# Kernel optimization log

Hardware: AMD Instinct MI355X
Metric: run time of the kernel (lower is better)

## Reference

```python
import jax, jax.numpy as jnp
import numpy as np

B, T, S = 32, 32, 400
H, E = 512, 300
V, MAX_OOV = 45000, 50
EXT_V = V + MAX_OOV
NEG = 1.0e12  # INF constant from the torch module


def setup_inputs() -> dict:
    key = jax.random.key(0)
    ks = jax.random.split(key, 16)
    p = lambda k, shape: jax.random.normal(k, shape, jnp.float32) * 0.02
    ext = jax.random.randint(ks[0], (B, S), 0, EXT_V, dtype=jnp.int64 if jax.config.jax_enable_x64 else jnp.int32)
    ext = ext.at[0, 0].set(EXT_V - 1)  # pin max OOV id so num_oov == MAX_OOV (matches torch data-dependent size)
    return {
        "trg_seq_embedded": jax.random.normal(ks[1], (B, T, E), jnp.float32),
        "ext_src_seq": ext,
        "init_states": jax.random.normal(ks[2], (1, B, H), jnp.float32),
        "encoder_outputs": jax.random.normal(ks[3], (B, S, H), jnp.float32),
        "encoder_mask": jnp.ones((B, S), jnp.int32),
        "W_enc": p(ks[4], (H, H)), "b_enc": jnp.zeros((H,), jnp.float32),
        "W_red": p(ks[5], (E, E + H)), "b_red": jnp.zeros((E,), jnp.float32),
        "W_ih": p(ks[6], (4 * H, E)), "W_hh": p(ks[7], (4 * H, H)),
        "b_ih": jnp.zeros((4 * H,), jnp.float32), "b_hh": jnp.zeros((4 * H,), jnp.float32),
        "W_cat": p(ks[8], (H, 2 * H)), "b_cat": jnp.zeros((H,), jnp.float32),
        "W_log": p(ks[9], (V, H)), "b_log": jnp.zeros((V,), jnp.float32),
    }


def reference(trg_seq_embedded, ext_src_seq, init_states, encoder_outputs, encoder_mask,
              W_enc, b_enc, W_red, b_red, W_ih, W_hh, b_ih, b_hh, W_cat, b_cat, W_log, b_log):
    batch = trg_seq_embedded.shape[0]
    # encoder features (memories): [B, S, H]
    memories = jnp.einsum('bsh,gh->bsg', encoder_outputs, W_enc) + b_enc
    batch_idx = jnp.arange(batch)[:, None]
    bias = b_ih + b_hh

    def step(carry, emb):
        h, c, ctx, cov = carry
        # reduce_layer on [embedded ; prev_context] -> [B, E]
        x = jnp.concatenate([emb, ctx], axis=-1) @ W_red.T + b_red
        # single-layer LSTM cell, torch gate order i,f,g,o
        gates = x @ W_ih.T + h @ W_hh.T + bias
        i_g, f_g, g_g, o_g = jnp.split(gates, 4, axis=-1)
        c_new = jax.nn.sigmoid(f_g) * c + jax.nn.sigmoid(i_g) * jnp.tanh(g_g)
        h_new = jax.nn.sigmoid(o_g) * jnp.tanh(c_new)
        # Bahdanau-style dot attention
        energy = jnp.einsum('bh,bsh->bs', h_new, memories)
        energy = jnp.where(encoder_mask == 0, -NEG, energy)
        attn = jax.nn.softmax(energy, axis=1)
        context = jnp.einsum('bs,bsh->bh', attn, memories)
        # output projection
        logit_in = jnp.tanh(jnp.concatenate([h_new, context], axis=-1) @ W_cat.T + b_cat)
        logit = logit_in @ W_log.T + b_log  # [B, V]
        # pointer: scatter_max of energies into extended vocabulary
        ext_logit = jnp.concatenate([logit, jnp.zeros((batch, EXT_V - V), logit.dtype)], axis=1)
        out = jnp.full((batch, EXT_V), -NEG, logit.dtype).at[batch_idx, ext_src_seq].max(energy)
        out = jnp.where(out == -NEG, 0.0, out)
        logit2 = ext_logit + out
        logit2 = jnp.where(logit2 == 0.0, -NEG, logit2)
        return (h_new, c_new, context, cov + attn), (logit2, attn, cov, energy)

    h0 = init_states[0]
    carry0 = (h0, h0, jnp.zeros((batch, memories.shape[-1]), trg_seq_embedded.dtype),
              jnp.zeros((batch, memories.shape[1]), trg_seq_embedded.dtype))
    _, (logits, attn_out, cov_out, energies) = jax.lax.scan(
        step, carry0, jnp.swapaxes(trg_seq_embedded, 0, 1))
    # each stacked over time: logits [T,B,EXT_V], attn/coverage/energies [T,B,S]
    return logits, attn_out, cov_out, energies
```

## Files before the change

kernel.cpp:

```cpp
#include <hip/hip_runtime.h>
#include <hip/hip_bf16.h>

typedef _Float16 h2 __attribute__((ext_vector_type(2)));
typedef _Float16 h8 __attribute__((ext_vector_type(8)));
typedef __attribute__((ext_vector_type(4))) float floatx4;

#define NEGF 1.0e12f

#if __has_builtin(__builtin_amdgcn_fdot2)
#define DOT2(a,b,c) __builtin_amdgcn_fdot2((a),(b),(c),false)
#else
static __device__ __forceinline__ float DOT2(h2 a, h2 b, float c){
  return c + (float)a[0]*(float)b[0] + (float)a[1]*(float)b[1];
}
#endif

__device__ __forceinline__ float dot8(h8 a, h8 b, float c){
  h2 a0 = {a[0],a[1]}, a1 = {a[2],a[3]}, a2 = {a[4],a[5]}, a3 = {a[6],a[7]};
  h2 b0 = {b[0],b[1]}, b1 = {b[2],b[3]}, b2 = {b[4],b[5]}, b3 = {b[6],b[7]};
  c = DOT2(a0,b0,c); c = DOT2(a1,b1,c); c = DOT2(a2,b2,c); c = DOT2(a3,b3,c);
  return c;
}

__device__ __forceinline__ unsigned f16bits(float x){
  union { _Float16 h; unsigned short u; } cv; cv.h = (_Float16)x; return (unsigned)cv.u;
}

#define GLD_LDS16(g, l) __builtin_amdgcn_global_load_lds( \
    (const __attribute__((address_space(1))) void*)(g),   \
    (__attribute__((address_space(3))) void*)(l), 16, 0, 0)

#define ALOAD64(p)    __hip_atomic_load((p), __ATOMIC_RELAXED, __HIP_MEMORY_SCOPE_AGENT)
#define ASTORE32(p,v) __hip_atomic_store((p), (v), __ATOMIC_RELAXED, __HIP_MEMORY_SCOPE_AGENT)

template<int EPI>
__global__ __launch_bounds__(256) void gemm_f16(
    const _Float16* __restrict__ A, const _Float16* __restrict__ B,
    float* __restrict__ Cf, _Float16* __restrict__ Ch,
    const float* __restrict__ bias, int N, int K, int ldc, int ntn)
{
  __shared__ char smem[32768];
  _Float16* Al = (_Float16*)smem;
  _Float16* Bl = (_Float16*)(smem + 16384);
  int bid = blockIdx.x;
  int bn = bid % ntn, bm = bid / ntn;
  int t = threadIdx.x;
  int w = t >> 6, l = t & 63;

  floatx4 acc[4][4];
#pragma unroll
  for (int i = 0; i < 4; ++i)
#pragma unroll
    for (int j = 0; j < 4; ++j) acc[i][j] = (floatx4){0.f, 0.f, 0.f, 0.f};

  const char* Ab = (const char*)A + (size_t)bm * 128 * K * 2;
  const char* Bb = (const char*)B + (size_t)bn * 128 * K * 2;
  const int rowb = K * 2;
  const int r0 = t >> 3;
  const int cbyte = ((t & 7) * 16) ^ (((t >> 3) & 7) << 4);
  char* AlB = (char*)Al;
  char* BlB = (char*)Bl;
  const int wm = (w >> 1) * 64, wn = (w & 1) * 64;

  for (int kt = 0; kt < K; kt += 64) {
    __syncthreads();
#pragma unroll
    for (int c = 0; c < 4; ++c) {
      int row = c * 32 + r0;
      GLD_LDS16(Ab + (size_t)row * rowb + kt * 2 + cbyte, AlB + c * 4096 + t * 16);
      GLD_LDS16(Bb + (size_t)row * rowb + kt * 2 + cbyte, BlB + c * 4096 + t * 16);
    }
    __syncthreads();
#pragma unroll
    for (int kk = 0; kk < 64; kk += 32) {
      h8 af[4], bfv[4];
#pragma unroll
      for (int i = 0; i < 4; ++i) {
        int ra = wm + i * 16 + (l & 15);
        int cb = ((kk << 1) + ((l >> 4) << 4)) ^ ((ra & 7) << 4);
        af[i] = *(const h8*)(AlB + ra * 128 + cb);
      }
#pragma unroll
      for (int j = 0; j < 4; ++j) {
        int ra = wn + j * 16 + (l & 15);
        int cb = ((kk << 1) + ((l >> 4) << 4)) ^ ((ra & 7) << 4);
        bfv[j] = *(const h8*)(BlB + ra * 128 + cb);
      }
#pragma unroll
      for (int i = 0; i < 4; ++i)
#pragma unroll
        for (int j = 0; j < 4; ++j)
          acc[i][j] = __builtin_amdgcn_mfma_f32_16x16x32_f16(af[i], bfv[j], acc[i][j], 0, 0, 0);
    }
  }

  if (EPI == 3) {
    float* Cs = (float*)smem;
#pragma unroll
    for (int half = 0; half < 2; ++half) {
      __syncthreads();
      if ((w >> 1) == half) {
        int rbase = ((l >> 4) << 2);
#pragma unroll
        for (int i = 0; i < 4; ++i)
#pragma unroll
          for (int j = 0; j < 4; ++j)
#pragma unroll
            for (int r = 0; r < 4; ++r)
              Cs[(i * 16 + rbase + r) * 128 + wn + j * 16 + (l & 15)] = acc[i][j][r];
      }
      __syncthreads();
#pragma unroll
      for (int rr = 0; rr < 16; ++rr) {
        int row = rr * 4 + w;
        int grow = bm * 128 + half * 64 + row;
        int cc = bn * 128 + 2 * l;
        float2 v = *(float2*)&Cs[row * 128 + 2 * l];
        float vv0, vv1;
        if (cc < N)     { float x0 = v.x + bias[cc];     vv0 = (x0 == 0.f) ? -NEGF : x0; } else vv0 = -NEGF;
        if (cc + 1 < N) { float x1 = v.y + bias[cc + 1]; vv1 = (x1 == 0.f) ? -NEGF : x1; } else vv1 = -NEGF;
        float* orow = Cf + (size_t)grow * ldc;
        if (cc + 1 < ldc) { float2 o; o.x = vv0; o.y = vv1; *(float2*)(orow + cc) = o; }
        else if (cc < ldc) orow[cc] = vv0;
      }
    }
  } else {
    int mbase = bm * 128 + wm + ((l >> 4) << 2);
    int nbase = bn * 128 + wn + (l & 15);
#pragma unroll
    for (int j = 0; j < 4; ++j) {
      int col = nbase + j * 16;
#pragma unroll
      for (int i = 0; i < 4; ++i) {
#pragma unroll
        for (int r = 0; r < 4; ++r) {
          int row = mbase + i * 16 + r;
          float v = acc[i][j][r];
          if (col < N) {
            float bv = bias ? bias[col] : 0.f;
            if (EPI == 0)      Cf[(size_t)row * ldc + col] = v + bv;
            else if (EPI == 1) Ch[(size_t)row * ldc + col] = (_Float16)(v + bv);
            else               Ch[(size_t)row * ldc + col] = (_Float16)tanhf(v + bv);
          }
        }
      }
    }
  }
}

__global__ void cast_pad_kernel(const float* __restrict__ src, _Float16* __restrict__ dst,
                                int R, int C, int ld_src, int Cpad, int ld_dst, long total){
  long i = (long)blockIdx.x * 256 + threadIdx.x;
  if (i >= total) return;
  int r = (int)(i / Cpad), c = (int)(i % Cpad);
  float v = (r < R && c < C) ? src[(size_t)r * ld_src + c] : 0.f;
  dst[(size_t)r * ld_dst + c] = (_Float16)v;
}

__global__ void cast_emb_kernel(const float* __restrict__ trg, _Float16* __restrict__ dst){
  int i = blockIdx.x * 256 + threadIdx.x;
  if (i >= 1024 * 320) return;
  int m = i / 320, e = i % 320;
  int tt = m >> 5, b = m & 31;
  float v = (e < 300) ? trg[((size_t)b * 32 + tt) * 300 + e] : 0.f;
  dst[i] = (_Float16)v;
}

__global__ void cast_wr2t_kernel(const float* __restrict__ wred, _Float16* __restrict__ dst){
  int i = blockIdx.x * 256 + threadIdx.x;
  if (i >= 512 * 320) return;
  int h = i / 320, e = i % 320;
  float v = (e < 300) ? wred[(size_t)e * 812 + 300 + h] : 0.f;
  dst[i] = (_Float16)v;
}

__global__ void init_kernel(const float* __restrict__ h0, const float* __restrict__ b_ih,
                            const float* __restrict__ b_hh,
                            _Float16* __restrict__ HCzT, float* __restrict__ bias_sum,
                            _Float16* __restrict__ X1h, unsigned* __restrict__ bar){
  int i = blockIdx.x * 256 + threadIdx.x;
  if (i < 32768) {
    int unit = i >> 3, pos = i & 7;
    int kc = unit >> 5, b = unit & 31;
    int k = kc * 8 + pos;
    HCzT[i] = (k < 512) ? (_Float16)h0[b * 512 + k] : (_Float16)0.f;
  }
  if (i < 2048)  bias_sum[i] = b_ih[i] + b_hh[i];
  if (i < 327680) X1h[i] = (_Float16)0.f;
  if (i < 1024) bar[i] = 0u;
}

__device__ __forceinline__ void gbar(unsigned* cnt){
  asm volatile("s_waitcnt vmcnt(0)" ::: "memory");
  __syncthreads();
  if (threadIdx.x == 0) {
    __hip_atomic_fetch_add(cnt, 1u, __ATOMIC_RELAXED, __HIP_MEMORY_SCOPE_AGENT);
    while (__hip_atomic_load(cnt, __ATOMIC_RELAXED, __HIP_MEMORY_SCOPE_AGENT) < 32u)
      __builtin_amdgcn_s_sleep(1);
  }
  __syncthreads();
  asm volatile("" ::: "memory");
}

__global__ __launch_bounds__(512, 1) void fused_loop(
    const _Float16* __restrict__ memh, _Float16* __restrict__ HCzT,
    _Float16* __restrict__ HC_A, const _Float16* __restrict__ Wz,
    const float* __restrict__ P, const float* __restrict__ inits,
    const int* __restrict__ mask, float* __restrict__ e_out,
    float* __restrict__ a_out, float* __restrict__ c_out, unsigned* __restrict__ bar)
{
  __shared__ char smem[32768];
  __shared__ float es[400];
  __shared__ float red[16];
  __shared__ float cum[400];
  __shared__ _Float16 hh[512];

  float* gl = (float*)smem;
  const int q = blockIdx.x, t = threadIdx.x;
  const int w = t >> 6, l = t & 63;
  const int mw = w >> 2, nw = w & 3;

  if (t < 400) cum[t] = 0.f;

  float creg = inits[(t >> 4) * 512 + q * 16 + (t & 15)];
  const _Float16* mb = memh + (size_t)q * 400 * 512;

  const _Float16* wbase[4];
#pragma unroll
  for (int s = 0; s < 4; ++s)
    wbase[s] = Wz + (size_t)(s * 512 + q * 16 + (l & 15)) * 1024 + nw * 256 + ((l >> 4) << 3);

  __syncthreads();

  for (int ts = 0; ts < 32; ++ts) {
    {
      unsigned long long* zsrc = (unsigned long long*)(HCzT + (size_t)ts * 32768);
      floatx4 acc[4];
#pragma unroll
      for (int s = 0; s < 4; ++s) acc[s] = (floatx4){0.f, 0.f, 0.f, 0.f};
#pragma unroll
      for (int kk8 = 0; kk8 < 8; ++kk8) {
        int unit = ((nw * 8 + kk8) * 4 + (l >> 4)) * 32 + mw * 16 + (l & 15);
        union { unsigned long long u[2]; h8 v; } za;
        za.u[0] = ALOAD64(zsrc + (size_t)unit * 2);
        za.u[1] = ALOAD64(zsrc + (size_t)unit * 2 + 1);
#pragma unroll
        for (int s = 0; s < 4; ++s) {
          h8 wv = *(const h8*)(wbase[s] + kk8 * 32);
          acc[s] = __builtin_amdgcn_mfma_f32_16x16x32_f16(za.v, wv, acc[s], 0, 0, 0);
        }
      }
#pragma unroll
      for (int s = 0; s < 4; ++s)
#pragma unroll
        for (int r = 0; r < 4; ++r) {
          int b = mw * 16 + ((l >> 4) << 2) + r;
          gl[(s * 4 + nw) * 512 + b * 16 + (l & 15)] = acc[s][r];
        }
    }
    __syncthreads();
    {
      int b = t >> 4, j16 = t & 15;
      const float* Pr = P + ((size_t)ts * 32 + b) * 2048 + q * 16 + j16;
      float g4[4];
#pragma unroll
      for (int s = 0; s < 4; ++s)
        g4[s] = gl[(s * 4 + 0) * 512 + t] + gl[(s * 4 + 1) * 512 + t]
              + gl[(s * 4 + 2) * 512 + t] + gl[(s * 4 + 3) * 512 + t] + Pr[s * 512];
      float ig = 1.f / (1.f + expf(-g4[0]));
      float fg = 1.f / (1.f + expf(-g4[1]));
      float og = 1.f / (1.f + expf(-g4[3]));
      float cn = fg * creg + ig * tanhf(g4[2]);
      float hn = og * tanhf(cn);
      creg = cn;
      unsigned hu = f16bits(hn);
      unsigned other = __shfl_xor(hu, 1);
      if (!(t & 1)) {
        unsigned pack = hu | (other << 16);
        int j = q * 16 + j16;
        unsigned* dst = (unsigned*)((char*)(HCzT + (size_t)(ts + 1) * 32768)
                                    + (((j >> 3) * 32 + b) << 4) + ((j & 7) << 1));
        ASTORE32(dst, pack);
        *(unsigned*)(HC_A + ((size_t)ts * 32 + b) * 1024 + j) = pack;
      }
    }
    gbar(bar + ts * 32);

    size_t obase = (size_t)ts * 12800 + q * 400;
    {
      if (t < 64) {
        unsigned long long* hsrc = (unsigned long long*)(HCzT + (size_t)(ts + 1) * 32768);
        union { unsigned long long u[2]; h8 v; } ha;
        ha.u[0] = ALOAD64(hsrc + ((size_t)t * 32 + q) * 2);
        ha.u[1] = ALOAD64(hsrc + ((size_t)t * 32 + q) * 2 + 1);
        *(h8*)&hh[t * 8] = ha.v;
      }
      __syncthreads();

      {
        int g = l >> 2, c = l & 3;
#pragma unroll
        for (int r = 0; r < 4; ++r) {
          int sr = r * 16 + g;
          if (sr < 50) {
            int s = w * 50 + sr;
            const _Float16* row = mb + (size_t)s * 512 + c * 128;
            float e = 0.f;
#pragma unroll
            for (int k = 0; k < 16; ++k)
              e = dot8(*(const h8*)(row + k * 8), *(const h8*)&hh[c * 128 + k * 8], e);
            e += __shfl_xor(e, 1);
            e += __shfl_xor(e, 2);
            if (c == 0) {
              if (mask[q * 400 + s] == 0) e = -NEGF;
              es[s] = e;
            }
          }
        }
      }
      __syncthreads();
      if (t < 400) e_out[obase + t] = es[t];

      float v = (t < 400) ? es[t] : -3.4e38f;
      float m = v;
#pragma unroll
      for (int o = 32; o; o >>= 1) m = fmaxf(m, __shfl_xor(m, o));
      if (l == 0) red[w] = m;
      __syncthreads();
      m = red[0];
#pragma unroll
      for (int qq = 1; qq < 8; ++qq) m = fmaxf(m, red[qq]);
      float p = (t < 400) ? expf(v - m) : 0.f;
      float sum = p;
#pragma unroll
      for (int o = 32; o; o >>= 1) sum += __shfl_xor(sum, o);
      if (l == 0) red[8 + w] = sum;
      __syncthreads();
      float tot = red[8];
#pragma unroll
      for (int qq = 9; qq < 16; ++qq) tot += red[qq];
      float inv = 1.f / tot;
      float aval = p * inv;
      if (t < 400) {
        es[t] = aval;
        a_out[obase + t] = aval;
        c_out[obase + t] = cum[t];
        cum[t] += aval;
      }
      __syncthreads();

      float acc2 = 0.f;
#pragma unroll 4
      for (int s = 0; s < 400; ++s)
        acc2 += es[s] * (float)mb[(size_t)s * 512 + t];
      unsigned cu = f16bits(acc2);
      unsigned other = __shfl_xor(cu, 1);
      if (!(t & 1)) {
        unsigned pack = cu | (other << 16);
        int kg = 512 + t;
        unsigned* dst = (unsigned*)((char*)(HCzT + (size_t)(ts + 1) * 32768)
                                    + (((kg >> 3) * 32 + q) << 4) + ((kg & 7) << 1));
        ASTORE32(dst, pack);
        *(unsigned*)(HC_A + ((size_t)ts * 32 + q) * 1024 + kg) = pack;
      }
    }
    gbar(bar + ts * 32 + 16);
  }
}

__global__ __launch_bounds__(512) void pointer_kernel(
    const int* __restrict__ ext, const float* __restrict__ energ, float* __restrict__ logits)
{
  __shared__ int ids[400];
  __shared__ float es[400];
  int tb = blockIdx.x;
  int b = tb & 31;
  int tt = tb >> 5;
  int t = threadIdx.x;
  if (t < 400) {
    ids[t] = ext[b * 400 + t];
    es[t] = energ[(size_t)tt * 12800 + b * 400 + t];
  }
  __syncthreads();
  if (t < 400) {
    int id = ids[t];
    bool first = true;
    for (int s = 0; s < t; ++s) if (ids[s] == id) { first = false; break; }
    if (first) {
      float mx = es[t];
      for (int s = t + 1; s < 400; ++s) if (ids[s] == id) mx = fmaxf(mx, es[s]);
      if (mx != -NEGF) {
        float* p = &logits[(size_t)tb * 45050 + id];
        float base = 0.f;
        if (id < 45000) { float cur = *p; base = (cur == -NEGF) ? 0.f : cur; }
        float nv = base + mx;
        *p = (nv == 0.f) ? -NEGF : nv;
      }
    }
  }
}

extern "C" void kernel_launch(void* const* d_in, const int* in_sizes, int n_in,
                              void* d_out, int out_size, void* d_ws, size_t ws_size,
                              hipStream_t stream) {
  const float* trg   = (const float*)d_in[0];
  const int*   ext   = (const int*)d_in[1];
  const float* inits = (const float*)d_in[2];
  const float* enc   = (const float*)d_in[3];
  const int*   mask  = (const int*)d_in[4];
  const float* W_enc = (const float*)d_in[5];
  const float* b_enc = (const float*)d_in[6];
  const float* W_red = (const float*)d_in[7];
  const float* b_red = (const float*)d_in[8];
  const float* W_ih  = (const float*)d_in[9];
  const float* W_hh  = (const float*)d_in[10];
  const float* b_ih  = (const float*)d_in[11];
  const float* b_hh  = (const float*)d_in[12];
  const float* W_cat = (const float*)d_in[13];
  const float* b_cat = (const float*)d_in[14];
  const float* W_log = (const float*)d_in[15];
  const float* b_log = (const float*)d_in[16];

  float* out = (float*)d_out;
  float* out_logits = out;
  float* out_attn   = out + 46131200;
  float* out_cov    = out_attn + 409600;
  float* out_energy = out_cov + 409600;

  char* ws = (char*)d_ws;
  size_t o = 0;
  auto alloc = [&](size_t bytes) { void* p = ws + o; o += (bytes + 255) & ~(size_t)255; return p; };
  _Float16* mem_h   = (_Float16*)alloc(12800ULL * 512 * 2);
  _Float16* enc_h   = (_Float16*)alloc(12800ULL * 512 * 2);
  _Float16* W_enc_h = (_Float16*)alloc(512ULL * 512 * 2);
  _Float16* emb_h   = (_Float16*)alloc(1024ULL * 320 * 2);
  _Float16* Wr1_h   = (_Float16*)alloc(384ULL * 320 * 2);
  _Float16* X1_h    = (_Float16*)alloc(1024ULL * 320 * 2);
  _Float16* W_ih_h  = (_Float16*)alloc(2048ULL * 320 * 2);
  _Float16* Wr2T_h  = (_Float16*)alloc(512ULL * 320 * 2);
  _Float16* W_cat_h = (_Float16*)alloc(512ULL * 1024 * 2);
  _Float16* W_log_h = (_Float16*)alloc(45056ULL * 512 * 2);
  _Float16* A_log_h = (_Float16*)alloc(1024ULL * 512 * 2);
  _Float16* HCzT    = (_Float16*)alloc(33ULL * 32768 * 2);
  _Float16* HC_A    = (_Float16*)alloc(1024ULL * 1024 * 2);
  _Float16* Wz      = (_Float16*)alloc(2048ULL * 1024 * 2);
  float* P        = (float*)alloc(1024ULL * 2048 * 4);
  float* bias_sum = (float*)alloc(2048ULL * 4);
  unsigned* bar   = (unsigned*)alloc(4096);

  auto blocks = [](long total) { return (int)((total + 255) / 256); };

  init_kernel<<<blocks(327680), 256, 0, stream>>>(inits, b_ih, b_hh, HCzT, bias_sum, X1_h, bar);
  cast_pad_kernel<<<blocks(12800L*512), 256, 0, stream>>>(enc,   enc_h,   12800, 512, 512, 512, 512, 12800L*512);
  cast_pad_kernel<<<blocks(512L*512),   256, 0, stream>>>(W_enc, W_enc_h, 512,   512, 512, 512, 512, 512L*512);
  cast_pad_kernel<<<blocks(384L*320),   256, 0, stream>>>(W_red, Wr1_h,   300,   300, 812, 320, 320, 384L*320);
  cast_pad_kernel<<<blocks(2048L*320),  256, 0, stream>>>(W_ih,  W_ih_h,  2048,  300, 300, 320, 320, 2048L*320);
  cast_pad_kernel<<<blocks(512L*1024),  256, 0, stream>>>(W_cat, W_cat_h, 512,  1024, 1024, 1024, 1024, 512L*1024);
  cast_pad_kernel<<<blocks(45056L*512), 256, 0, stream>>>(W_log, W_log_h, 45000, 512, 512, 512, 512, 45056L*512);
  cast_pad_kernel<<<blocks(2048L*512),  256, 0, stream>>>(W_hh,  Wz,      2048,  512, 512, 512, 1024, 2048L*512);
  cast_emb_kernel<<<blocks(1024L*320), 256, 0, stream>>>(trg, emb_h);
  cast_wr2t_kernel<<<blocks(512L*320), 256, 0, stream>>>(W_red, Wr2T_h);

  gemm_f16<1><<<400, 256, 0, stream>>>(enc_h, W_enc_h, nullptr, mem_h, b_enc, 512, 512, 512, 4);
  gemm_f16<1><<<24,  256, 0, stream>>>(emb_h, Wr1_h, nullptr, X1_h, b_red, 300, 320, 320, 3);
  gemm_f16<0><<<128, 256, 0, stream>>>(X1_h, W_ih_h, P, nullptr, bias_sum, 2048, 320, 2048, 16);
  gemm_f16<1><<<64,  256, 0, stream>>>(W_ih_h, Wr2T_h, nullptr, Wz + 512, nullptr, 512, 320, 1024, 4);

  fused_loop<<<32, 512, 0, stream>>>(mem_h, HCzT, HC_A, Wz, P, inits, mask,
                                     out_energy, out_attn, out_cov, bar);

  gemm_f16<2><<<32, 256, 0, stream>>>(HC_A, W_cat_h, nullptr, A_log_h, b_cat, 512, 1024, 512, 4);
  gemm_f16<3><<<2816, 256, 0, stream>>>(A_log_h, W_log_h, out_logits, nullptr, b_log, 45000, 512, 45050, 352);
  pointer_kernel<<<1024, 512, 0, stream>>>(ext, out_energy, out_logits);
}
```

Before: 1.393 ms.

## Transpose encoder memories for vectorized context reduction and use flag-based grid barrier

Adds a transpose kernel that writes the encoder memories in [b][h][s] layout, reusing the enc_h buffer. Each thread in the recurrent loop can then compute the attention context with contiguous 16-byte loads and vectorized shared-memory reads, instead of strided scalar loads. The grid barrier moves from a single atomic counter to per-block generation flags, polled in parallel by one wavefront with a ballot, to shorten barrier latency. The cost is one extra transpose launch and more global reads per barrier poll.

```diff
diff --git a/kernel.cpp b/kernel.cpp
--- a/kernel.cpp
+++ b/kernel.cpp
@@ -174,6 +174,34 @@
   dst[i] = (_Float16)v;
 }
 
+__global__ __launch_bounds__(256) void transpose_mem(
+    const _Float16* __restrict__ src, _Float16* __restrict__ dst)
+{
+  __shared__ _Float16 tile[64][66];
+  int bid = blockIdx.x;
+  int b = bid / 56, rem = bid % 56;
+  int st = rem / 8, dt = rem % 8;
+  int t = threadIdx.x;
+  int lane = t & 63, grp = t >> 6;
+  const _Float16* s0 = src + (size_t)b * 400 * 512;
+#pragma unroll
+  for (int j = 0; j < 16; ++j) {
+    int sl = grp * 16 + j;
+    int s = st * 64 + sl;
+    if (s < 400) tile[sl][lane] = s0[(size_t)s * 512 + dt * 64 + lane];
+  }
+  __syncthreads();
+  _Float16* d0 = dst + (size_t)b * 512 * 400;
+  int s = st * 64 + lane;
+  if (s < 400) {
+#pragma unroll
+    for (int j = 0; j < 16; ++j) {
+      int dl = grp * 16 + j;
+      d0[(size_t)(dt * 64 + dl) * 400 + s] = tile[lane][dl];
+    }
+  }
+}
+
 __global__ void init_kernel(const float* __restrict__ h0, const float* __restrict__ b_ih,
                             const float* __restrict__ b_hh,
                             _Float16* __restrict__ HCzT, float* __restrict__ bias_sum,
@@ -190,27 +218,33 @@
   if (i < 1024) bar[i] = 0u;
 }
 
-__device__ __forceinline__ void gbar(unsigned* cnt){
+__device__ __forceinline__ void gbar2(unsigned* flags, unsigned gen){
   asm volatile("s_waitcnt vmcnt(0)" ::: "memory");
   __syncthreads();
-  if (threadIdx.x == 0) {
-    __hip_atomic_fetch_add(cnt, 1u, __ATOMIC_RELAXED, __HIP_MEMORY_SCOPE_AGENT);
-    while (__hip_atomic_load(cnt, __ATOMIC_RELAXED, __HIP_MEMORY_SCOPE_AGENT) < 32u)
-      __builtin_amdgcn_s_sleep(1);
+  if (threadIdx.x < 64) {
+    if (threadIdx.x == 0)
+      __hip_atomic_store(flags + blockIdx.x, gen, __ATOMIC_RELAXED, __HIP_MEMORY_SCOPE_AGENT);
+    for (;;) {
+      unsigned v = (threadIdx.x < 32)
+        ? __hip_atomic_load(flags + threadIdx.x, __ATOMIC_RELAXED, __HIP_MEMORY_SCOPE_AGENT)
+        : gen;
+      if (__ballot(v >= gen) == ~0ULL) break;
+    }
   }
   __syncthreads();
   asm volatile("" ::: "memory");
 }
 
 __global__ __launch_bounds__(512, 1) void fused_loop(
-    const _Float16* __restrict__ memh, _Float16* __restrict__ HCzT,
-    _Float16* __restrict__ HC_A, const _Float16* __restrict__ Wz,
-    const float* __restrict__ P, const float* __restrict__ inits,
-    const int* __restrict__ mask, float* __restrict__ e_out,
-    float* __restrict__ a_out, float* __restrict__ c_out, unsigned* __restrict__ bar)
+    const _Float16* __restrict__ memh, const _Float16* __restrict__ memT,
+    _Float16* __restrict__ HCzT, _Float16* __restrict__ HC_A,
+    const _Float16* __restrict__ Wz, const float* __restrict__ P,
+    const float* __restrict__ inits, const int* __restrict__ mask,
+    float* __restrict__ e_out, float* __restrict__ a_out,
+    float* __restrict__ c_out, unsigned* __restrict__ bar)
 {
   __shared__ char smem[32768];
-  __shared__ float es[400];
+  __shared__ __align__(16) float es[400];
   __shared__ float red[16];
   __shared__ float cum[400];
   __shared__ _Float16 hh[512];
@@ -224,6 +258,7 @@
 
   float creg = inits[(t >> 4) * 512 + q * 16 + (t & 15)];
   const _Float16* mb = memh + (size_t)q * 400 * 512;
+  const _Float16* rowT = memT + (size_t)q * 204800 + (size_t)t * 400;
 
   const _Float16* wbase[4];
 #pragma unroll
@@ -284,7 +319,7 @@
         *(unsigned*)(HC_A + ((size_t)ts * 32 + b) * 1024 + j) = pack;
       }
     }
-    gbar(bar + ts * 32);
+    gbar2(bar, ts + 1);
 
     size_t obase = (size_t)ts * 12800 + q * 400;
     {
@@ -350,9 +385,16 @@
       __syncthreads();
 
       float acc2 = 0.f;
-#pragma unroll 4
-      for (int s = 0; s < 400; ++s)
-        acc2 += es[s] * (float)mb[(size_t)s * 512 + t];
+#pragma unroll
+      for (int si = 0; si < 50; ++si) {
+        h8 mv = *(const h8*)(rowT + si * 8);
+        float4 ea = *(const float4*)&es[si * 8];
+        float4 eb = *(const float4*)&es[si * 8 + 4];
+        acc2 += ea.x * (float)mv[0] + ea.y * (float)mv[1]
+              + ea.z * (float)mv[2] + ea.w * (float)mv[3]
+              + eb.x * (float)mv[4] + eb.y * (float)mv[5]
+              + eb.z * (float)mv[6] + eb.w * (float)mv[7];
+      }
       unsigned cu = f16bits(acc2);
       unsigned other = __shfl_xor(cu, 1);
       if (!(t & 1)) {
@@ -364,7 +406,7 @@
         *(unsigned*)(HC_A + ((size_t)ts * 32 + q) * 1024 + kg) = pack;
       }
     }
-    gbar(bar + ts * 32 + 16);
+    gbar2(bar + 32, ts + 1);
   }
 }
 
@@ -447,6 +489,7 @@
   float* P        = (float*)alloc(1024ULL * 2048 * 4);
   float* bias_sum = (float*)alloc(2048ULL * 4);
   unsigned* bar   = (unsigned*)alloc(4096);
+  _Float16* memT  = enc_h;
 
   auto blocks = [](long total) { return (int)((total + 255) / 256); };
 
@@ -466,7 +509,9 @@
   gemm_f16<0><<<128, 256, 0, stream>>>(X1_h, W_ih_h, P, nullptr, bias_sum, 2048, 320, 2048, 16);
   gemm_f16<1><<<64,  256, 0, stream>>>(W_ih_h, Wr2T_h, nullptr, Wz + 512, nullptr, 512, 320, 1024, 4);
 
-  fused_loop<<<32, 512, 0, stream>>>(mem_h, HCzT, HC_A, Wz, P, inits, mask,
+  transpose_mem<<<32 * 56, 256, 0, stream>>>(mem_h, memT);
+
+  fused_loop<<<32, 512, 0, stream>>>(mem_h, memT, HCzT, HC_A, Wz, P, inits, mask,
                                      out_energy, out_attn, out_cov, bar);
 
   gemm_f16<2><<<32, 256, 0, stream>>>(HC_A, W_cat_h, nullptr, A_log_h, b_cat, 512, 1024, 512, 4);
```

New measurement: 1.647 ms. 18.3% more time.

## Replace grid-barrier LSTM split with per-batch blocks computing full gates

Applied to the files above, without the earlier changes.

Restructures the recurrent loop so each block handles one batch element and computes all LSTM gates locally with fp16 dot products over a repacked weight layout. This removes the two grid-wide atomic barriers per timestep and the global h/context exchange buffer. In exchange, every block streams the full recurrent weight matrix each step instead of a slice, which greatly increases cache/memory traffic. Block size doubles to 1024 threads and the context reduction is split into two halves.

```diff
diff --git a/kernel.cpp b/kernel.cpp
--- a/kernel.cpp
+++ b/kernel.cpp
@@ -22,16 +22,9 @@
   return c;
 }
 
-__device__ __forceinline__ unsigned f16bits(float x){
-  union { _Float16 h; unsigned short u; } cv; cv.h = (_Float16)x; return (unsigned)cv.u;
-}
-
 #define GLD_LDS16(g, l) __builtin_amdgcn_global_load_lds( \
     (const __attribute__((address_space(1))) void*)(g),   \
     (__attribute__((address_space(3))) void*)(l), 16, 0, 0)
-
-#define ALOAD64(p)    __hip_atomic_load((p), __ATOMIC_RELAXED, __HIP_MEMORY_SCOPE_AGENT)
-#define ASTORE32(p,v) __hip_atomic_store((p), (v), __ATOMIC_RELAXED, __HIP_MEMORY_SCOPE_AGENT)
 
 template<int EPI>
 __global__ __launch_bounds__(256) void gemm_f16(
@@ -174,197 +167,152 @@
   dst[i] = (_Float16)v;
 }
 
-__global__ void init_kernel(const float* __restrict__ h0, const float* __restrict__ b_ih,
-                            const float* __restrict__ b_hh,
-                            _Float16* __restrict__ HCzT, float* __restrict__ bias_sum,
-                            _Float16* __restrict__ X1h, unsigned* __restrict__ bar){
+__global__ void repack_w(const _Float16* __restrict__ Wz, _Float16* __restrict__ Wblk){
+  int idx = blockIdx.x * 256 + threadIdx.x;
+  if (idx >= 262144) return;
+  int kb = idx >> 11, j = idx & 2047;
+  *(h8*)(Wblk + (size_t)idx * 8) = *(const h8*)(Wz + (size_t)j * 1024 + kb * 8);
+}
+
+__global__ void init_kernel(const float* __restrict__ b_ih, const float* __restrict__ b_hh,
+                            float* __restrict__ bias_sum, _Float16* __restrict__ X1h){
   int i = blockIdx.x * 256 + threadIdx.x;
-  if (i < 32768) {
-    int unit = i >> 3, pos = i & 7;
-    int kc = unit >> 5, b = unit & 31;
-    int k = kc * 8 + pos;
-    HCzT[i] = (k < 512) ? (_Float16)h0[b * 512 + k] : (_Float16)0.f;
-  }
   if (i < 2048)  bias_sum[i] = b_ih[i] + b_hh[i];
   if (i < 327680) X1h[i] = (_Float16)0.f;
-  if (i < 1024) bar[i] = 0u;
-}
-
-__device__ __forceinline__ void gbar(unsigned* cnt){
-  asm volatile("s_waitcnt vmcnt(0)" ::: "memory");
-  __syncthreads();
-  if (threadIdx.x == 0) {
-    __hip_atomic_fetch_add(cnt, 1u, __ATOMIC_RELAXED, __HIP_MEMORY_SCOPE_AGENT);
-    while (__hip_atomic_load(cnt, __ATOMIC_RELAXED, __HIP_MEMORY_SCOPE_AGENT) < 32u)
-      __builtin_amdgcn_s_sleep(1);
-  }
-  __syncthreads();
-  asm volatile("" ::: "memory");
-}
-
-__global__ __launch_bounds__(512, 1) void fused_loop(
-    const _Float16* __restrict__ memh, _Float16* __restrict__ HCzT,
-    _Float16* __restrict__ HC_A, const _Float16* __restrict__ Wz,
+}
+
+__global__ __launch_bounds__(1024, 1) void fused_loop(
+    const _Float16* __restrict__ memh, const _Float16* __restrict__ Wblk,
     const float* __restrict__ P, const float* __restrict__ inits,
-    const int* __restrict__ mask, float* __restrict__ e_out,
-    float* __restrict__ a_out, float* __restrict__ c_out, unsigned* __restrict__ bar)
+    const int* __restrict__ mask, _Float16* __restrict__ HC_A,
+    float* __restrict__ e_out, float* __restrict__ a_out, float* __restrict__ c_out)
 {
-  __shared__ char smem[32768];
-  __shared__ float es[400];
-  __shared__ float red[16];
+  __shared__ __align__(16) _Float16 zl[1024];
+  __shared__ float gl[2048];
+  __shared__ __align__(16) float es[400];
   __shared__ float cum[400];
-  __shared__ _Float16 hh[512];
-
-  float* gl = (float*)smem;
+  __shared__ float red[32];
+  __shared__ float part[512];
+  __shared__ int msk[400];
+
   const int q = blockIdx.x, t = threadIdx.x;
   const int w = t >> 6, l = t & 63;
-  const int mw = w >> 2, nw = w & 3;
-
-  if (t < 400) cum[t] = 0.f;
-
-  float creg = inits[(t >> 4) * 512 + q * 16 + (t & 15)];
   const _Float16* mb = memh + (size_t)q * 400 * 512;
 
-  const _Float16* wbase[4];
-#pragma unroll
-  for (int s = 0; s < 4; ++s)
-    wbase[s] = Wz + (size_t)(s * 512 + q * 16 + (l & 15)) * 1024 + nw * 256 + ((l >> 4) << 3);
-
+  if (t < 400) { cum[t] = 0.f; msk[t] = mask[q * 400 + t]; }
+  float creg = 0.f;
+  if (t < 512) {
+    float h0 = inits[q * 512 + t];
+    creg = h0;
+    zl[t] = (_Float16)h0;
+    zl[512 + t] = (_Float16)0.f;
+  }
   __syncthreads();
 
   for (int ts = 0; ts < 32; ++ts) {
     {
-      unsigned long long* zsrc = (unsigned long long*)(HCzT + (size_t)ts * 32768);
-      floatx4 acc[4];
-#pragma unroll
-      for (int s = 0; s < 4; ++s) acc[s] = (floatx4){0.f, 0.f, 0.f, 0.f};
-#pragma unroll
-      for (int kk8 = 0; kk8 < 8; ++kk8) {
-        int unit = ((nw * 8 + kk8) * 4 + (l >> 4)) * 32 + mw * 16 + (l & 15);
-        union { unsigned long long u[2]; h8 v; } za;
-        za.u[0] = ALOAD64(zsrc + (size_t)unit * 2);
-        za.u[1] = ALOAD64(zsrc + (size_t)unit * 2 + 1);
-#pragma unroll
-        for (int s = 0; s < 4; ++s) {
-          h8 wv = *(const h8*)(wbase[s] + kk8 * 32);
-          acc[s] = __builtin_amdgcn_mfma_f32_16x16x32_f16(za.v, wv, acc[s], 0, 0, 0);
-        }
-      }
-#pragma unroll
-      for (int s = 0; s < 4; ++s)
-#pragma unroll
-        for (int r = 0; r < 4; ++r) {
-          int b = mw * 16 + ((l >> 4) << 2) + r;
-          gl[(s * 4 + nw) * 512 + b * 16 + (l & 15)] = acc[s][r];
-        }
-    }
-    __syncthreads();
-    {
-      int b = t >> 4, j16 = t & 15;
-      const float* Pr = P + ((size_t)ts * 32 + b) * 2048 + q * 16 + j16;
-      float g4[4];
-#pragma unroll
-      for (int s = 0; s < 4; ++s)
-        g4[s] = gl[(s * 4 + 0) * 512 + t] + gl[(s * 4 + 1) * 512 + t]
-              + gl[(s * 4 + 2) * 512 + t] + gl[(s * 4 + 3) * 512 + t] + Pr[s * 512];
-      float ig = 1.f / (1.f + expf(-g4[0]));
-      float fg = 1.f / (1.f + expf(-g4[1]));
-      float og = 1.f / (1.f + expf(-g4[3]));
-      float cn = fg * creg + ig * tanhf(g4[2]);
+      float a0 = 0.f, b0 = 0.f, a1 = 0.f, b1 = 0.f;
+      const _Float16* wp = Wblk + (size_t)t * 8;
+#pragma unroll 4
+      for (int kb = 0; kb < 128; kb += 2) {
+        h8 zv0 = *(const h8*)&zl[kb * 8];
+        h8 zv1 = *(const h8*)&zl[kb * 8 + 8];
+        const _Float16* w0p = wp + (size_t)kb * 16384;
+        a0 = dot8(*(const h8*)(w0p), zv0, a0);
+        a1 = dot8(*(const h8*)(w0p + 8192), zv0, a1);
+        b0 = dot8(*(const h8*)(w0p + 16384), zv1, b0);
+        b1 = dot8(*(const h8*)(w0p + 16384 + 8192), zv1, b1);
+      }
+      gl[t] = a0 + b0;
+      gl[1024 + t] = a1 + b1;
+    }
+    __syncthreads();
+    if (t < 512) {
+      const float* Pr = P + ((size_t)ts * 32 + q) * 2048 + t;
+      float gi = gl[t]        + Pr[0];
+      float gf = gl[512 + t]  + Pr[512];
+      float gg = gl[1024 + t] + Pr[1024];
+      float go = gl[1536 + t] + Pr[1536];
+      float ig = 1.f / (1.f + expf(-gi));
+      float fg = 1.f / (1.f + expf(-gf));
+      float og = 1.f / (1.f + expf(-go));
+      float cn = fg * creg + ig * tanhf(gg);
       float hn = og * tanhf(cn);
       creg = cn;
-      unsigned hu = f16bits(hn);
-      unsigned other = __shfl_xor(hu, 1);
-      if (!(t & 1)) {
-        unsigned pack = hu | (other << 16);
-        int j = q * 16 + j16;
-        unsigned* dst = (unsigned*)((char*)(HCzT + (size_t)(ts + 1) * 32768)
-                                    + (((j >> 3) * 32 + b) << 4) + ((j & 7) << 1));
-        ASTORE32(dst, pack);
-        *(unsigned*)(HC_A + ((size_t)ts * 32 + b) * 1024 + j) = pack;
-      }
-    }
-    gbar(bar + ts * 32);
-
-    size_t obase = (size_t)ts * 12800 + q * 400;
+      zl[t] = (_Float16)hn;
+      HC_A[((size_t)ts * 32 + q) * 1024 + t] = (_Float16)hn;
+    }
+    __syncthreads();
+
     {
-      if (t < 64) {
-        unsigned long long* hsrc = (unsigned long long*)(HCzT + (size_t)(ts + 1) * 32768);
-        union { unsigned long long u[2]; h8 v; } ha;
-        ha.u[0] = ALOAD64(hsrc + ((size_t)t * 32 + q) * 2);
-        ha.u[1] = ALOAD64(hsrc + ((size_t)t * 32 + q) * 2 + 1);
-        *(h8*)&hh[t * 8] = ha.v;
-      }
-      __syncthreads();
-
-      {
-        int g = l >> 2, c = l & 3;
-#pragma unroll
-        for (int r = 0; r < 4; ++r) {
-          int sr = r * 16 + g;
-          if (sr < 50) {
-            int s = w * 50 + sr;
-            const _Float16* row = mb + (size_t)s * 512 + c * 128;
-            float e = 0.f;
-#pragma unroll
-            for (int k = 0; k < 16; ++k)
-              e = dot8(*(const h8*)(row + k * 8), *(const h8*)&hh[c * 128 + k * 8], e);
-            e += __shfl_xor(e, 1);
-            e += __shfl_xor(e, 2);
-            if (c == 0) {
-              if (mask[q * 400 + s] == 0) e = -NEGF;
-              es[s] = e;
-            }
+      int g = l >> 2, c = l & 3;
+#pragma unroll
+      for (int r = 0; r < 2; ++r) {
+        int sr = r * 16 + g;
+        if (sr < 25) {
+          int s = w * 25 + sr;
+          const _Float16* row = mb + (size_t)s * 512 + c * 128;
+          float e = 0.f;
+#pragma unroll
+          for (int k = 0; k < 16; ++k)
+            e = dot8(*(const h8*)(row + k * 8), *(const h8*)&zl[c * 128 + k * 8], e);
+          e += __shfl_xor(e, 1);
+          e += __shfl_xor(e, 2);
+          if (c == 0) {
+            if (msk[s] == 0) e = -NEGF;
+            es[s] = e;
           }
         }
       }
+    }
+    __syncthreads();
+    size_t obase = (size_t)ts * 12800 + q * 400;
+    if (t < 400) e_out[obase + t] = es[t];
+
+    float v = (t < 400) ? es[t] : -3.4e38f;
+    float m = v;
+#pragma unroll
+    for (int o = 32; o; o >>= 1) m = fmaxf(m, __shfl_xor(m, o));
+    if (l == 0) red[w] = m;
+    __syncthreads();
+    m = red[0];
+#pragma unroll
+    for (int qq = 1; qq < 16; ++qq) m = fmaxf(m, red[qq]);
+    float p = (t < 400) ? expf(v - m) : 0.f;
+    float sum = p;
+#pragma unroll
+    for (int o = 32; o; o >>= 1) sum += __shfl_xor(sum, o);
+    if (l == 0) red[16 + w] = sum;
+    __syncthreads();
+    float tot = red[16];
+#pragma unroll
+    for (int qq = 17; qq < 32; ++qq) tot += red[qq];
+    float inv = 1.f / tot;
+    float aval = p * inv;
+    if (t < 400) {
+      es[t] = aval;
+      a_out[obase + t] = aval;
+      c_out[obase + t] = cum[t];
+      cum[t] += aval;
+    }
+    __syncthreads();
+
+    {
+      int col = t & 511, half = t >> 9;
+      int s0 = half * 200;
+      float acc = 0.f;
+#pragma unroll 4
+      for (int si = 0; si < 200; ++si)
+        acc += es[s0 + si] * (float)mb[(size_t)(s0 + si) * 512 + col];
+      if (half == 0) part[col] = acc;
       __syncthreads();
-      if (t < 400) e_out[obase + t] = es[t];
-
-      float v = (t < 400) ? es[t] : -3.4e38f;
-      float m = v;
-#pragma unroll
-      for (int o = 32; o; o >>= 1) m = fmaxf(m, __shfl_xor(m, o));
-      if (l == 0) red[w] = m;
-      __syncthreads();
-      m = red[0];
-#pragma unroll
-      for (int qq = 1; qq < 8; ++qq) m = fmaxf(m, red[qq]);
-      float p = (t < 400) ? expf(v - m) : 0.f;
-      float sum = p;
-#pragma unroll
-      for (int o = 32; o; o >>= 1) sum += __shfl_xor(sum, o);
-      if (l == 0) red[8 + w] = sum;
-      __syncthreads();
-      float tot = red[8];
-#pragma unroll
-      for (int qq = 9; qq < 16; ++qq) tot += red[qq];
-      float inv = 1.f / tot;
-      float aval = p * inv;
-      if (t < 400) {
-        es[t] = aval;
-        a_out[obase + t] = aval;
-        c_out[obase + t] = cum[t];
-        cum[t] += aval;
-      }
-      __syncthreads();
-
-      float acc2 = 0.f;
-#pragma unroll 4
-      for (int s = 0; s < 400; ++s)
-        acc2 += es[s] * (float)mb[(size_t)s * 512 + t];
-      unsigned cu = f16bits(acc2);
-      unsigned other = __shfl_xor(cu, 1);
-      if (!(t & 1)) {
-        unsigned pack = cu | (other << 16);
-        int kg = 512 + t;
-        unsigned* dst = (unsigned*)((char*)(HCzT + (size_t)(ts + 1) * 32768)
-                                    + (((kg >> 3) * 32 + q) << 4) + ((kg & 7) << 1));
-        ASTORE32(dst, pack);
-        *(unsigned*)(HC_A + ((size_t)ts * 32 + q) * 1024 + kg) = pack;
-      }
-    }
-    gbar(bar + ts * 32 + 16);
+      if (half == 1) {
+        float cv = part[col] + acc;
+        zl[512 + col] = (_Float16)cv;
+        HC_A[((size_t)ts * 32 + q) * 1024 + 512 + col] = (_Float16)cv;
+      }
+    }
+    __syncthreads();
   }
 }
 
@@ -441,16 +389,15 @@
   _Float16* W_cat_h = (_Float16*)alloc(512ULL * 1024 * 2);
   _Float16* W_log_h = (_Float16*)alloc(45056ULL * 512 * 2);
   _Float16* A_log_h = (_Float16*)alloc(1024ULL * 512 * 2);
-  _Float16* HCzT    = (_Float16*)alloc(33ULL * 32768 * 2);
   _Float16* HC_A    = (_Float16*)alloc(1024ULL * 1024 * 2);
   _Float16* Wz      = (_Float16*)alloc(2048ULL * 1024 * 2);
+  _Float16* Wblk    = (_Float16*)alloc(2048ULL * 1024 * 2);
   float* P        = (float*)alloc(1024ULL * 2048 * 4);
   float* bias_sum = (float*)alloc(2048ULL * 4);
-  unsigned* bar   = (unsigned*)alloc(4096);
 
   auto blocks = [](long total) { return (int)((total + 255) / 256); };
 
-  init_kernel<<<blocks(327680), 256, 0, stream>>>(inits, b_ih, b_hh, HCzT, bias_sum, X1_h, bar);
+  init_kernel<<<blocks(327680), 256, 0, stream>>>(b_ih, b_hh, bias_sum, X1_h);
   cast_pad_kernel<<<blocks(12800L*512), 256, 0, stream>>>(enc,   enc_h,   12800, 512, 512, 512, 512, 12800L*512);
   cast_pad_kernel<<<blocks(512L*512),   256, 0, stream>>>(W_enc, W_enc_h, 512,   512, 512, 512, 512, 512L*512);
   cast_pad_kernel<<<blocks(384L*320),   256, 0, stream>>>(W_red, Wr1_h,   300,   300, 812, 320, 320, 384L*320);
@@ -466,8 +413,10 @@
   gemm_f16<0><<<128, 256, 0, stream>>>(X1_h, W_ih_h, P, nullptr, bias_sum, 2048, 320, 2048, 16);
   gemm_f16<1><<<64,  256, 0, stream>>>(W_ih_h, Wr2T_h, nullptr, Wz + 512, nullptr, 512, 320, 1024, 4);
 
-  fused_loop<<<32, 512, 0, stream>>>(mem_h, HCzT, HC_A, Wz, P, inits, mask,
-                                     out_energy, out_attn, out_cov, bar);
+  repack_w<<<1024, 256, 0, stream>>>(Wz, Wblk);
+
+  fused_loop<<<32, 1024, 0, stream>>>(mem_h, Wblk, P, inits, mask, HC_A,
+                                      out_energy, out_attn, out_cov);
 
   gemm_f16<2><<<32, 256, 0, stream>>>(HC_A, W_cat_h, nullptr, A_log_h, b_cat, 512, 1024, 512, 4);
   gemm_f16<3><<<2816, 256, 0, stream>>>(A_log_h, W_log_h, out_logits, nullptr, b_log, 45000, 512, 45050, 352);
```

Result: slower. 3.655 ms (+162.4%).
